# Kernel optimization log

Hardware: AMD Instinct MI355X
Metric: run time of the kernel (lower is better)

The kernel has to match this reference:

```python
import jax, jax.numpy as jnp
from jax import lax
import numpy as np

NF = 64   # nf
T = 7     # in_nc == 2*radius+1 frames
KS = 3    # deform kernel size
K = KS * KS


def conv2d(x, w, b, stride=1, pad=1):
    out = lax.conv_general_dilated(x, w, (stride, stride), [(pad, pad), (pad, pad)],
                                   dimension_numbers=('NCHW', 'OIHW', 'NCHW'))
    return out + b[None, :, None, None]


def convT2d(x, w, b):
    # torch ConvTranspose2d(k=4, stride=2, padding=1); w: (Cin, Cout, 4, 4)
    wf = jnp.flip(w, (2, 3)).transpose(1, 0, 2, 3)
    out = lax.conv_general_dilated(x, wf, (1, 1), [(2, 2), (2, 2)], lhs_dilation=(2, 2),
                                   dimension_numbers=('NCHW', 'OIHW', 'NCHW'))
    return out + b[None, :, None, None]


def bilinear_gather(img, ys, xs):
    # img: (C, H, W); ys/xs: (...,) absolute pixel coords; zero padding outside
    C, H, W = img.shape
    y0 = jnp.floor(ys); x0 = jnp.floor(xs)
    wy = ys - y0; wx = xs - x0

    def tap(yi, xi, wgt):
        valid = (yi >= 0) & (yi <= H - 1) & (xi >= 0) & (xi <= W - 1)
        yc = jnp.clip(yi, 0, H - 1).astype(jnp.int32)
        xc = jnp.clip(xi, 0, W - 1).astype(jnp.int32)
        return img[:, yc, xc] * (wgt * valid.astype(img.dtype))

    return (tap(y0, x0, (1 - wy) * (1 - wx)) + tap(y0, x0 + 1, (1 - wy) * wx)
            + tap(y0 + 1, x0, wy * (1 - wx)) + tap(y0 + 1, x0 + 1, wy * wx))


def flow_warp(x, flow):
    # x: (C, H, W); flow: (H, W, 2) with (dx, dy); align_corners=True grid_sample
    # with the normalization in the torch code reduces to absolute-pixel bilinear.
    H, W = x.shape[-2:]
    gy, gx = jnp.meshgrid(jnp.arange(H, dtype=x.dtype), jnp.arange(W, dtype=x.dtype), indexing='ij')
    return bilinear_gather(x, gy + flow[..., 1], gx + flow[..., 0])


def mod_deform_conv(x, off, msk, w, b):
    # Modulated deformable conv v2; deformable_groups = Cin (1 channel per group).
    B, Cin, H, W = x.shape
    G = Cin
    off = off.reshape(B, G, K, 2, H, W)   # per-group (dy, dx) per kernel tap
    msk = msk.reshape(B, G, K, H, W)
    gy, gx = jnp.meshgrid(jnp.arange(H, dtype=x.dtype), jnp.arange(W, dtype=x.dtype), indexing='ij')
    kk = jnp.arange(K)
    ky = (kk // KS - KS // 2).astype(x.dtype)
    kx = (kk % KS - KS // 2).astype(x.dtype)
    ys = gy[None, None, None] + ky[None, None, :, None, None] + off[:, :, :, 0]  # (B,G,K,H,W)
    xs = gx[None, None, None] + kx[None, None, :, None, None] + off[:, :, :, 1]
    xg = x.reshape(B, G, 1, H, W)
    samp = jax.vmap(jax.vmap(jax.vmap(bilinear_gather, in_axes=(None, 0, 0)),
                             in_axes=(0, 0, 0)), in_axes=(0, 0, 0))(xg, ys, xs)
    # samp: (B, G, K, 1, H, W)
    mod = samp * msk[:, :, :, None]
    wk = w.reshape(w.shape[0], G, 1, K)   # (O, G, Cpg=1, K)
    out = jnp.einsum('bgkchw,ogck->bohw', mod, wk)
    return out + b[None, :, None, None]


def _agg(feats, aligned, pred, ff_w, ff_b, dn1_w, dn1_b, dn2_w, dn2_b,
         tr_cw, tr_cb, tr_tw, tr_tb, up1_cw, up1_cb, up1_tw, up1_tb,
         up2_cw, up2_cb, up2_tw, up2_tb):
    B, T_, C, H, W = feats.shape
    ref = feats[:, T_ // 2][:, None]                      # center frame embedding
    p1 = jax.nn.sigmoid(aligned * ref)
    p2 = jax.nn.sigmoid(pred * ref)
    a1 = (aligned * p1).reshape(B, T_ * C, H, W)
    a2 = (pred * p2).reshape(B, T_ * C, H, W)
    f = feats.reshape(B, T_ * C, H, W)
    fuse = lambda z: jax.nn.leaky_relu(conv2d(z, ff_w, ff_b), 0.1)
    out0 = 0.1 * fuse(a1 + a2) + fuse(f)
    out1 = jax.nn.relu(conv2d(out0, dn1_w, dn1_b, stride=2))
    out2 = jax.nn.relu(conv2d(out1, dn2_w, dn2_b, stride=2))
    out = jax.nn.relu(convT2d(jax.nn.relu(conv2d(out2, tr_cw, tr_cb, stride=2)), tr_tw, tr_tb))
    out = jax.nn.relu(convT2d(jax.nn.relu(conv2d(jnp.concatenate([out, out2], 1), up2_cw, up2_cb)), up2_tw, up2_tb))
    out = jax.nn.relu(convT2d(jax.nn.relu(conv2d(jnp.concatenate([out, out1], 1), up1_cw, up1_cb)), up1_tw, up1_tb))
    return out


def _forward(lqs, preds, mv, bw1, bb1, bw2, bb2, dn1_w, dn1_b, dn2_w, dn2_b,
             up1_cw, up1_cb, up1_tw, up1_tb, up2_cw, up2_cb, up2_tw, up2_tb,
             tr_cw, tr_cb, tr_tw, tr_tb, ff_w, ff_b, om_w, om_b, dc_w, dc_b):
    B, T_, H, W = lqs.shape
    bb = lambda z: conv2d(conv2d(z, bw1, bb1), bw2, bb2)
    feat = bb(lqs.reshape(B * T_, 1, H, W)).reshape(B, T_, NF, H, W)
    pred_feat = bb(preds).reshape(B, T_, NF, H, W)
    # alg_MV_fea[:,0] = feat[:,0]; alg_MV_fea[:,i] = warp(feat[:,i-1], mv[:,i-1])
    prev = feat[:, :T_ - 1].reshape(B * (T_ - 1), NF, H, W)
    flows = mv.reshape(B * (T_ - 1), H, W, 2)
    warped = jax.vmap(flow_warp)(prev, flows).reshape(B, T_ - 1, NF, H, W)
    alg = jnp.concatenate([feat[:, :1], warped], axis=1)
    feat_f = _agg(feat, alg, pred_feat, ff_w, ff_b, dn1_w, dn1_b, dn2_w, dn2_b,
                  tr_cw, tr_cb, tr_tw, tr_tb, up1_cw, up1_cb, up1_tw, up1_tb,
                  up2_cw, up2_cb, up2_tw, up2_tb)
    off_msk = conv2d(feat_f, om_w, om_b)      # (B, T*3*K, H, W)
    n_off = T_ * 2 * K
    off = off_msk[:, :n_off]
    m = jax.nn.sigmoid(off_msk[:, n_off:])
    return jax.nn.relu(mod_deform_conv(lqs, off, m, dc_w, dc_b))


def setup_inputs():
    key = jax.random.key(0)
    ks = iter(jax.random.split(key, 40))
    B, H, W = 1, 192, 192
    r = lambda shape: jax.random.normal(next(ks), shape, jnp.float32)
    w = lambda shape: r(shape) * 0.05
    return {
        'lqs': r((B, T, H, W)),
        'preds': r((B * T, 1, H, W)),
        'mv': r((B, T - 1, H, W, 2)),
        'bw1': w((NF, 1, 3, 3)), 'bb1': w((NF,)),
        'bw2': w((NF, NF, 3, 3)), 'bb2': w((NF,)),
        'dn1_w': w((NF, NF, 3, 3)), 'dn1_b': w((NF,)),
        'dn2_w': w((NF, NF, 3, 3)), 'dn2_b': w((NF,)),
        'up1_cw': w((NF, 2 * NF, 3, 3)), 'up1_cb': w((NF,)),
        'up1_tw': w((NF, NF, 4, 4)), 'up1_tb': w((NF,)),
        'up2_cw': w((NF, 2 * NF, 3, 3)), 'up2_cb': w((NF,)),
        'up2_tw': w((NF, NF, 4, 4)), 'up2_tb': w((NF,)),
        'tr_cw': w((NF, NF, 3, 3)), 'tr_cb': w((NF,)),
        'tr_tw': w((NF, NF, 4, 4)), 'tr_tb': w((NF,)),
        'ff_w': w((NF, T * NF, 3, 3)), 'ff_b': w((NF,)),
        'om_w': w((T * 3 * K, NF, 3, 3)), 'om_b': w((T * 3 * K,)),
        'dc_w': w((NF, T, 3, 3)), 'dc_b': w((NF,)),
    }


def reference(lqs, preds, mv, bw1, bb1, bw2, bb2, dn1_w, dn1_b, dn2_w, dn2_b,
              up1_cw, up1_cb, up1_tw, up1_tb, up2_cw, up2_cb, up2_tw, up2_tb,
              tr_cw, tr_cb, tr_tw, tr_tb, ff_w, ff_b, om_w, om_b, dc_w, dc_b):
    return _forward(lqs, preds, mv, bw1, bb1, bw2, bb2, dn1_w, dn1_b, dn2_w, dn2_b,
                    up1_cw, up1_cb, up1_tw, up1_tb, up2_cw, up2_cb, up2_tw, up2_tb,
                    tr_cw, tr_cb, tr_tw, tr_tb, ff_w, ff_b, om_w, om_b, dc_w, dc_b)
```

## Files before the change

kernel.cpp:

```cpp
#include <hip/hip_runtime.h>
#include <math.h>

#define IMH 192
#define IMW 192
#define HWF 36864
#define PDIM 194

typedef unsigned short u16t;
typedef __attribute__((ext_vector_type(8))) short short8;
typedef __attribute__((ext_vector_type(4))) float f32x4;

__device__ __forceinline__ float sigmoidf(float x){ return 1.f/(1.f+expf(-x)); }
__device__ __forceinline__ float lrelu(float x){ return x > 0.f ? x : 0.1f*x; }
__device__ __forceinline__ float b2f(u16t h){ unsigned u = ((unsigned)h)<<16; return __uint_as_float(u); }
__device__ __forceinline__ u16t f2b(float f){
  unsigned u = __float_as_uint(f);
  u += 0x7FFFu + ((u>>16)&1u);
  return (u16t)(u>>16);
}

__device__ __forceinline__ float bilin(const float* __restrict__ img, float ys, float xs, int H, int W){
  float y0f = floorf(ys), x0f = floorf(xs);
  float wy = ys - y0f, wx = xs - x0f;
  int y0 = (int)y0f, x0 = (int)x0f;
  float acc = 0.f;
  #pragma unroll
  for (int dy=0; dy<2; ++dy){
    int yi = y0+dy;
    float wyv = dy ? wy : 1.f-wy;
    if (yi < 0 || yi >= H) continue;
    #pragma unroll
    for (int dx=0; dx<2; ++dx){
      int xi = x0+dx;
      float wxv = dx ? wx : 1.f-wx;
      if (xi < 0 || xi >= W) continue;
      acc += img[yi*W+xi]*(wyv*wxv);
    }
  }
  return acc;
}

struct PkD { const float* w; u16t* dst; int Cin, Cout, NT, total; };
struct PkD8 { PkD d[8]; };
__global__ __launch_bounds__(256) void pack_all(PkD8 ds){
  PkD d = ds.d[blockIdx.y];
  int id = blockIdx.x*256 + threadIdx.x;
  if (id >= d.total) return;
  int j = id & 7, l = (id>>3) & 63;
  int r = id >> 9;
  int nt = r % d.NT; r /= d.NT;
  int KC = d.Cin >> 5;
  int kc = r % KC; int tap = r / KC;
  int c = kc*32 + ((l>>4)<<3) + j;
  int o = nt*16 + (l&15);
  float v = (o < d.Cout) ? d.w[((size_t)o*d.Cin + c)*9 + tap] : 0.f;
  d.dst[id] = f2b(v);
}

struct RpD { const float* w; float* wp; };
struct RpD3 { RpD d[3]; };
__global__ __launch_bounds__(256) void repack_all(RpD3 ds){
  RpD d = ds.d[blockIdx.y];
  int id = blockIdx.x*256 + threadIdx.x;
  int par = id >> 12, o = (id >> 6) & 63, i = id & 63;
  int ry = par >> 1, rx = par & 1;
  #pragma unroll
  for (int jy = 0; jy < 2; ++jy)
    #pragma unroll
    for (int jx = 0; jx < 2; ++jx){
      int ka = 3 - ry - 2*jy, kb = 3 - rx - 2*jx;
      d.wp[((size_t)((par*64 + o)*64 + i))*4 + jy*2 + jx] = d.w[((size_t)(i*64 + o))*16 + ka*4 + kb];
    }
}

struct PzD { u16t* buf; int C, dim, nimg; size_t stride; };
struct PzD5 { PzD d[5]; };
__global__ __launch_bounds__(256) void padzero_all(PzD5 ds){
  PzD d = ds.d[blockIdx.y];
  int per = (4*d.dim - 4)*d.C;
  long total = (long)per*d.nimg;
  for (long id = (long)blockIdx.x*256 + threadIdx.x; id < total; id += (long)gridDim.x*256){
    int n = (int)(id / per), c2 = (int)(id % per);
    int cell = c2 / d.C, c = c2 % d.C;
    int d2 = d.dim - 1;
    int r, col;
    if (cell < d.dim){ r = 0; col = cell; }
    else if (cell < 2*d.dim){ r = d2; col = cell - d.dim; }
    else if (cell < 3*d.dim - 2){ r = cell - 2*d.dim + 1; col = 0; }
    else { r = cell - (3*d.dim - 2) + 1; col = d2; }
    d.buf[(size_t)n*d.stride + ((size_t)r*d.dim + col)*d.C + c] = 0;
  }
}

__global__ __launch_bounds__(256) void padzero2(u16t* buf, int C, int dim){
  int total = (4*dim - 4)*C;
  for (int id = blockIdx.x*256 + threadIdx.x; id < total; id += gridDim.x*256){
    int cell = id / C, c = id % C;
    int d2 = dim - 1;
    int r, col;
    if (cell < dim){ r = 0; col = cell; }
    else if (cell < 2*dim){ r = d2; col = cell - dim; }
    else if (cell < 3*dim - 2){ r = cell - 2*dim + 1; col = 0; }
    else { r = cell - (3*dim - 2) + 1; col = d2; }
    buf[((size_t)r*dim + col)*C + c] = 0;
  }
}

__global__ __launch_bounds__(256) void conv1_k(const float* __restrict__ lqs, const float* __restrict__ preds,
                                               const float* __restrict__ w,
                                               const float* __restrict__ bias, u16t* __restrict__ outp){
  __shared__ float sw[576];
  __shared__ float sb[64];
  int tid = threadIdx.x;
  for (int i = tid; i < 576; i += 256) sw[i] = w[i];
  if (tid < 64) sb[tid] = bias[tid];
  __syncthreads();
  int idx = blockIdx.x*256 + tid;
  int n = blockIdx.y;
  int y = idx/IMW, x = idx%IMW;
  const float* ip = (n < 7) ? (lqs + (size_t)n*HWF) : (preds + (size_t)(n-7)*HWF);
  float t[9];
  #pragma unroll
  for (int dy = 0; dy < 3; ++dy)
    #pragma unroll
    for (int dx = 0; dx < 3; ++dx){
      int yy = y+dy-1, xx = x+dx-1;
      t[dy*3+dx] = (yy>=0 && yy<IMH && xx>=0 && xx<IMW) ? ip[yy*IMW+xx] : 0.f;
    }
  u16t* op = outp + (size_t)n*(PDIM*PDIM*64) + ((size_t)(y+1)*PDIM + x+1)*64;
  #pragma unroll
  for (int o8 = 0; o8 < 8; ++o8){
    short8 ov;
    #pragma unroll
    for (int j = 0; j < 8; ++j){
      int o = o8*8 + j;
      float acc = sb[o];
      #pragma unroll
      for (int k = 0; k < 9; ++k) acc += t[k]*sw[o*9+k];
      ov[j] = (short)f2b(acc);
    }
    *(short8*)(op + o8*8) = ov;
  }
}

template<int STREAMS, int KC, int OMODE, int NTT, int SWZ>
__global__ __launch_bounds__(256) void cgemm(
    const u16t* __restrict__ A0, const u16t* __restrict__ A1,
    const u16t* __restrict__ Bp, const float* __restrict__ bias,
    float* __restrict__ outf, u16t* __restrict__ outb, u16t* __restrict__ outb2,
    int Cout, int blocksPerImg, int pitchIn, int csIn, size_t aImgStride, int KCtot)
{
  __shared__ u16t sA[STREAMS*108*40];
  int bid = blockIdx.x;
  if (SWZ) bid = (bid & 7)*(gridDim.x >> 3) + (bid >> 3);
  const int tid = threadIdx.x;
  const int wave = tid >> 6, lane = tid & 63;
  const int m = lane & 15, q = lane >> 4;
  const int img = bid / blocksPerImg;
  const int rem = bid - img*blocksPerImg;
  const int yg = rem / 12, xsg = rem % 12;
  const int y0 = yg*4, xs = xsg*16;
  const int rp = wave >> 1, np = wave & 1;
  const int ntB = (OMODE == 5) ? blockIdx.y*4 : 0;
  f32x4 acc[STREAMS][2][2];
  #pragma unroll
  for (int s = 0; s < STREAMS; ++s)
    #pragma unroll
    for (int r = 0; r < 2; ++r)
      #pragma unroll
      for (int n = 0; n < 2; ++n) acc[s][r][n] = (f32x4){0.f,0.f,0.f,0.f};

  #pragma unroll 1
  for (int kc = 0; kc < KC; ++kc){
    if (kc) __syncthreads();
    for (int u = tid; u < STREAMS*216; u += 256){
      int st = u/216, r2 = u%216, p = r2>>1, h = r2&1;
      int rr = p/18, cc = p%18;
      size_t ga = (size_t)img*aImgStride + ((size_t)(y0+rr)*pitchIn + xs+cc)*csIn + kc*32 + h*16;
      const u16t* gp = ((STREAMS==2 && st==1) ? A1 : A0) + ga;
      short8 v0 = *(const short8*)gp;
      short8 v1 = *(const short8*)(gp + 8);
      u16t* lp = &sA[((size_t)(st*108 + p))*40 + h*16];
      *(short8*)lp = v0;
      *(short8*)(lp+8) = v1;
    }
    __syncthreads();
    #pragma unroll
    for (int tap = 0; tap < 9; ++tap){
      const int dy = tap/3, dx = tap%3;
      short8 af[STREAMS][2];
      #pragma unroll
      for (int st = 0; st < STREAMS; ++st)
        #pragma unroll
        for (int r = 0; r < 2; ++r)
          af[st][r] = *(const short8*)&sA[((size_t)(st*108 + (2*rp + r + dy)*18 + dx + m))*40 + q*8];
      const u16t* bp = Bp + ((size_t)(tap*KCtot + kc)*NTT + ntB + np*2)*512 + lane*8;
      short8 b0 = *(const short8*)bp;
      short8 b1 = *(const short8*)(bp + 512);
      #pragma unroll
      for (int st = 0; st < STREAMS; ++st)
        #pragma unroll
        for (int r = 0; r < 2; ++r){
          acc[st][r][0] = __builtin_amdgcn_mfma_f32_16x16x32_bf16(af[st][r], b0, acc[st][r][0], 0, 0, 0);
          acc[st][r][1] = __builtin_amdgcn_mfma_f32_16x16x32_bf16(af[st][r], b1, acc[st][r][1], 0, 0, 0);
        }
    }
  }
  const int px0 = q*4;
  #pragma unroll
  for (int r = 0; r < 2; ++r){
    int yout = y0 + 2*rp + r;
    #pragma unroll
    for (int n = 0; n < 2; ++n){
      int oL = (np*2 + n)*16 + m;
      if (OMODE == 4){
        float bv = bias[oL];
        #pragma unroll
        for (int g = 0; g < 4; ++g){
          int px = xs + px0 + g;
          float v = 0.1f*lrelu(acc[0][r][n][g] + bv) + lrelu(acc[1][r][n][g] + bv);
          outb[((size_t)(yout+1)*PDIM + px+1)*64 + oL] = f2b(v);
        }
      } else if (OMODE == 5){
        int o = ntB*16 + oL;
        if (o < Cout){
          float bv = bias[o];
          #pragma unroll
          for (int g = 0; g < 4; ++g){
            int px = xs + px0 + g;
            outf[(size_t)o*HWF + (size_t)yout*IMW + px] = acc[0][r][n][g] + bv;
          }
        }
      } else {
        float bv = bias[oL];
        #pragma unroll
        for (int g = 0; g < 4; ++g){
          int px = xs + px0 + g;
          float v = acc[0][r][n][g] + bv;
          if (img < 7)
            outb[((size_t)(yout+1)*PDIM + px+1)*448 + (size_t)img*64 + oL] = f2b(v);
          else
            outb2[(size_t)(img-7)*((size_t)HWF*64) + ((size_t)yout*IMW + px)*64 + oL] = f2b(v);
        }
      }
    }
  }
}

template<int NT, int STREAMS, int KC, int STRIDE, int OMODE, int ACT, int SWZ>
__global__ __launch_bounds__(256) void gconv3(
    const u16t* __restrict__ A0, const u16t* __restrict__ A1,
    const u16t* __restrict__ Bp, const float* __restrict__ bias,
    float* __restrict__ outf, u16t* __restrict__ outb,
    int Cout, int Wout, int strips, int blocksPerImg,
    int pitchIn, int csIn, int coIn, size_t aImgStride,
    size_t outImgStride, int pitchOut, int csOut, int coOut,
    int KCtot, int NTtot)
{
  int bid = blockIdx.x;
  if (SWZ) bid = (bid & 7)*(gridDim.x >> 3) + (bid >> 3);
  const int wave = threadIdx.x >> 6;
  const int lane = threadIdx.x & 63;
  const int img = bid / blocksPerImg;
  const int sid = (bid - img*blocksPerImg)*4 + wave;
  const int y = sid / strips, xs = (sid % strips) * 16;
  const int m = lane & 15, q = lane >> 4;
  const int ntOff = blockIdx.y*NT;
  f32x4 acc[NT];
  #pragma unroll
  for (int nt = 0; nt < NT; ++nt) acc[nt] = (f32x4){0.f,0.f,0.f,0.f};

  for (int tap = 0; tap < 9; ++tap){
    int dy = tap/3, dx = tap%3;
    int row = STRIDE*y + dy;
    int col = (STRIDE == 1) ? (xs + m + dx) : (2*(xs + m) + dx);
    size_t abase = (size_t)img*aImgStride + ((size_t)row*pitchIn + col)*csIn + coIn + q*8;
    const u16t* ap0 = A0 + abase;
    const u16t* bp = Bp + ((size_t)(tap*KCtot)*NTtot + ntOff)*512 + lane*8;
    #pragma unroll
    for (int kc = 0; kc < KC; ++kc){
      short8 av0 = *(const short8*)(ap0 + kc*32);
      #pragma unroll
      for (int nt = 0; nt < NT; ++nt){
        short8 bv = *(const short8*)(bp + (size_t)(kc*NTtot + nt)*512);
        acc[nt] = __builtin_amdgcn_mfma_f32_16x16x32_bf16(av0, bv, acc[nt], 0, 0, 0);
      }
    }
  }
  const int prow0 = q*4;
  #pragma unroll
  for (int nt = 0; nt < NT; ++nt){
    int o = (ntOff + nt)*16 + m;
    if (o >= Cout) continue;
    float bv = bias[o];
    #pragma unroll
    for (int r = 0; r < 4; ++r){
      int px = xs + prow0 + r;
      if (px >= Wout) continue;
      float v = acc[nt][r] + bv;
      if (ACT) v = fmaxf(v, 0.f);
      if (OMODE == 0){
        outf[((size_t)img*Cout + o)*((size_t)Wout*Wout) + (size_t)y*Wout + px] = v;
      } else if (OMODE == 1){
        outb[(size_t)img*outImgStride + ((size_t)(y+1)*pitchOut + px+1)*csOut + coOut + o] = f2b(v);
      } else {
        outb[(size_t)img*outImgStride + ((size_t)y*pitchOut + px)*csOut + coOut + o] = f2b(v);
      }
    }
  }
}

__global__ __launch_bounds__(256) void gate_nhwc(
    const u16t* __restrict__ fpad, const u16t* __restrict__ pred,
    const float* __restrict__ mv, u16t* __restrict__ spad)
{
  int bid = blockIdx.x;
  int xcd = bid & 7;
  int k = bid >> 3;
  int t = k % 7;
  int lb = k / 7;
  int idx = (xcd*18 + lb)*256 + threadIdx.x;
  int y = idx/IMW, x = idx%IMW;
  size_t pc = ((size_t)(y+1)*PDIM + (x+1))*448;
  const u16t* rp = fpad + pc + 192;
  const u16t* pp = pred + ((size_t)t*HWF + idx)*64;
  u16t* sp = spad + pc + (size_t)t*64;
  const u16t* tp[4]; float tw[4];
  if (t == 0){
    tp[0] = fpad + pc; tw[0] = 1.f;
    tp[1] = tp[2] = tp[3] = fpad + pc; tw[1] = tw[2] = tw[3] = 0.f;
  } else {
    float fx = mv[(((size_t)(t-1)*HWF + idx))*2 + 0];
    float fy = mv[(((size_t)(t-1)*HWF + idx))*2 + 1];
    float ys = (float)y + fy, xs = (float)x + fx;
    float y0f = floorf(ys), x0f = floorf(xs);
    float wy = ys - y0f, wx = xs - x0f;
    int y0 = (int)y0f, x0i = (int)x0f;
    int kk = 0;
    #pragma unroll
    for (int dy2 = 0; dy2 < 2; ++dy2)
      #pragma unroll
      for (int dx2 = 0; dx2 < 2; ++dx2){
        int yi = y0+dy2, xi = x0i+dx2;
        float wv = (dy2 ? wy : 1.f-wy)*(dx2 ? wx : 1.f-wx);
        bool ok = (yi >= 0 && yi <= 191 && xi >= 0 && xi <= 191);
        int yc = min(max(yi,0),191), xc = min(max(xi,0),191);
        tp[kk] = fpad + ((size_t)(yc+1)*PDIM + xc+1)*448 + (size_t)(t-1)*64;
        tw[kk] = ok ? wv : 0.f;
        ++kk;
      }
  }
  #pragma unroll
  for (int c8 = 0; c8 < 8; ++c8){
    short8 rv = *(const short8*)(rp + c8*8);
    short8 pv = *(const short8*)(pp + c8*8);
    short8 t0v = *(const short8*)(tp[0] + c8*8);
    short8 t1v = *(const short8*)(tp[1] + c8*8);
    short8 t2v = *(const short8*)(tp[2] + c8*8);
    short8 t3v = *(const short8*)(tp[3] + c8*8);
    short8 ov;
    #pragma unroll
    for (int j = 0; j < 8; ++j){
      float r = b2f((u16t)rv[j]);
      float p = b2f((u16t)pv[j]);
      float a = tw[0]*b2f((u16t)t0v[j]) + tw[1]*b2f((u16t)t1v[j])
              + tw[2]*b2f((u16t)t2v[j]) + tw[3]*b2f((u16t)t3v[j]);
      float sv = a*sigmoidf(a*r) + p*sigmoidf(p*r);
      ov[j] = (short)f2b(sv);
    }
    *(short8*)(sp + c8*8) = ov;
  }
}

__global__ __launch_bounds__(256) void convT_tile2(
    const float* __restrict__ in, const float* __restrict__ wp,
    const float* __restrict__ bias, u16t* __restrict__ outb,
    int Hin, int tilesX, int pitchOut, int csOut, int coOut)
{
  const int CC = 4;
  __shared__ float sIn[CC][10*11];
  __shared__ float sW[16][CC][4][4];
  const int Win = Hin;
  const int o0 = blockIdx.x*16;
  const int tile = blockIdx.y;
  const int ty0 = (tile/tilesX)*16, tx0 = (tile%tilesX)*16;
  const int tid = threadIdx.x;
  const int py = tid>>4, px = tid&15;
  const int ry = py&1, rx = px&1, par = ry*2 + rx;
  const int lr = py>>1, lc = px>>1;
  const int r0 = ty0>>1, c0 = tx0>>1;
  float acc[16] = {};
  for (int ib = 0; ib < 64; ib += CC){
    for (int i = tid; i < CC*100; i += 256){
      int c = i/100, rem = i%100, r = rem/10, col = rem%10;
      int gy = r0 - 1 + r, gx = c0 - 1 + col;
      float v = 0.f;
      if (gy >= 0 && gy < Hin && gx >= 0 && gx < Win)
        v = in[(size_t)(ib + c)*Hin*Win + gy*Win + gx];
      sIn[c][r*11 + col] = v;
    }
    for (int i = tid; i < 1024; i += 256){
      int ol = i >> 6, rem = i & 63, ci = rem >> 4, p2 = (rem >> 2) & 3, j = rem & 3;
      sW[ol][ci][p2][j] = wp[((size_t)((p2*64 + o0 + ol)*64) + ib + ci)*4 + j];
    }
    __syncthreads();
    #pragma unroll
    for (int ci = 0; ci < CC; ++ci){
      int rb = lr + ry, cb = lc + rx;
      float t00 = sIn[ci][rb*11 + cb],     t01 = sIn[ci][rb*11 + cb + 1];
      float t10 = sIn[ci][(rb+1)*11 + cb], t11 = sIn[ci][(rb+1)*11 + cb + 1];
      #pragma unroll
      for (int ol = 0; ol < 16; ++ol){
        const float* wv = &sW[ol][ci][par][0];
        acc[ol] += t00*wv[0] + t01*wv[1] + t10*wv[2] + t11*wv[3];
      }
    }
    __syncthreads();
  }
  int gy = ty0 + py, gx = tx0 + px;
  u16t* op = outb + ((size_t)(gy+1)*pitchOut + gx+1)*csOut + coOut + o0;
  short8 pa, pb;
  #pragma unroll
  for (int i = 0; i < 8; ++i) pa[i] = (short)f2b(fmaxf(acc[i] + bias[o0+i], 0.f));
  #pragma unroll
  for (int i = 0; i < 8; ++i) pb[i] = (short)f2b(fmaxf(acc[8+i] + bias[o0+8+i], 0.f));
  *(short8*)op = pa;
  *(short8*)(op + 8) = pb;
}

__global__ __launch_bounds__(256) void deform_sample_k(
    const float* __restrict__ lqs, const float* __restrict__ om,
    float* __restrict__ vbuf)
{
  int idx = blockIdx.x*256 + threadIdx.x;
  int g = blockIdx.y;
  int h = idx / IMW, x = idx % IMW;
  const float* img = lqs + (size_t)g*HWF;
  #pragma unroll
  for (int k = 0; k < 9; ++k){
    int j = g*9 + k;
    float offy = om[(size_t)(j*2 + 0)*HWF + idx];
    float offx = om[(size_t)(j*2 + 1)*HWF + idx];
    float m = sigmoidf(om[(size_t)(126 + j)*HWF + idx]);
    float ys = (float)(h + (k/3) - 1) + offy;
    float xs = (float)(x + (k%3) - 1) + offx;
    vbuf[(size_t)j*HWF + idx] = bilin(img, ys, xs, IMH, IMW) * m;
  }
}

__global__ __launch_bounds__(256) void deform_out_k(
    const float* __restrict__ vbuf, const float* __restrict__ dcw,
    const float* __restrict__ dcb, float* __restrict__ out)
{
  __shared__ float sw[16*63];
  int idx = blockIdx.x*256 + threadIdx.x;
  int o0 = blockIdx.y*16;
  for (int i = threadIdx.x; i < 16*63; i += 256)
    sw[i] = dcw[(size_t)o0*63 + i];
  __syncthreads();
  float v[63];
  #pragma unroll
  for (int j = 0; j < 63; ++j) v[j] = vbuf[(size_t)j*HWF + idx];
  for (int ol = 0; ol < 16; ++ol){
    float acc = dcb[o0 + ol];
    #pragma unroll
    for (int j = 0; j < 63; ++j) acc += v[j]*sw[ol*63 + j];
    out[(size_t)(o0 + ol)*HWF + idx] = fmaxf(acc, 0.f);
  }
}

extern "C" void kernel_launch(void* const* d_in, const int* in_sizes, int n_in,
                              void* d_out, int out_size, void* d_ws, size_t ws_size,
                              hipStream_t stream)
{
  const float* lqs   = (const float*)d_in[0];
  const float* preds = (const float*)d_in[1];
  const float* mv    = (const float*)d_in[2];
  const float* bw1   = (const float*)d_in[3];
  const float* bb1   = (const float*)d_in[4];
  const float* bw2   = (const float*)d_in[5];
  const float* bb2   = (const float*)d_in[6];
  const float* dn1w  = (const float*)d_in[7];
  const float* dn1b  = (const float*)d_in[8];
  const float* dn2w  = (const float*)d_in[9];
  const float* dn2b  = (const float*)d_in[10];
  const float* up1cw = (const float*)d_in[11];
  const float* up1cb = (const float*)d_in[12];
  const float* up1tw = (const float*)d_in[13];
  const float* up1tb = (const float*)d_in[14];
  const float* up2cw = (const float*)d_in[15];
  const float* up2cb = (const float*)d_in[16];
  const float* up2tw = (const float*)d_in[17];
  const float* up2tb = (const float*)d_in[18];
  const float* trcw  = (const float*)d_in[19];
  const float* trcb  = (const float*)d_in[20];
  const float* trtw  = (const float*)d_in[21];
  const float* trtb  = (const float*)d_in[22];
  const float* ffw   = (const float*)d_in[23];
  const float* ffb   = (const float*)d_in[24];
  const float* omw   = (const float*)d_in[25];
  const float* omb   = (const float*)d_in[26];
  const float* dcw   = (const float*)d_in[27];
  const float* dcb   = (const float*)d_in[28];
  float* outp = (float*)d_out;

  char* p = (char*)d_ws;
  const size_t PIMG64 = (size_t)PDIM*PDIM*64;
  u16t* bbpad    = (u16t*)p; p += 14*PIMG64*2;
  u16t* fpad     = (u16t*)p; p += (size_t)PDIM*PDIM*448*2;
  u16t* prednhwc = (u16t*)p; p += (size_t)7*HWF*64*2;
  u16t* out0pad  = (u16t*)p; p += (size_t)PDIM*PDIM*64*2;
  u16t* cat1pad  = (u16t*)p; p += (size_t)98*98*128*2;
  u16t* cat2pad  = (u16t*)p; p += (size_t)50*50*128*2;
  float* t0      = (float*)p; p += (size_t)24*24*64*4;
  float* u2      = (float*)p; p += (size_t)48*48*64*4;
  float* u1      = (float*)p; p += (size_t)96*96*64*4;
  u16t* ffwpack  = (u16t*)p; p += 258048*2;
  u16t* c2pack   = (u16t*)p; p += 36864*2;
  u16t* ompack   = (u16t*)p; p += 110592*2;
  u16t* dn1pack  = (u16t*)p; p += 36864*2;
  u16t* dn2pack  = (u16t*)p; p += 36864*2;
  u16t* trcpack  = (u16t*)p; p += 36864*2;
  u16t* up2cpack = (u16t*)p; p += 73728*2;
  u16t* up1cpack = (u16t*)p; p += 73728*2;
  float* wp0     = (float*)p; p += 65536*4;
  float* wp1     = (float*)p; p += 65536*4;
  float* wp2     = (float*)p; p += 65536*4;

  u16t* spad = bbpad;
  u16t* featfpad = bbpad;
  float* om = (float*)prednhwc;
  float* vbuf = (float*)fpad;

  dim3 blk(256);
  PkD8 pk = {{ {ffw, ffwpack, 448, 64, 4, 258048}, {bw2, c2pack, 64, 64, 4, 36864},
               {omw, ompack, 64, 189, 12, 110592}, {dn1w, dn1pack, 64, 64, 4, 36864},
               {dn2w, dn2pack, 64, 64, 4, 36864},  {trcw, trcpack, 64, 64, 4, 36864},
               {up2cw, up2cpack, 128, 64, 4, 73728}, {up1cw, up1cpack, 128, 64, 4, 73728} }};
  pack_all<<<dim3(1008,8), blk, 0, stream>>>(pk);
  RpD3 rp3 = {{ {trtw, wp0}, {up2tw, wp1}, {up1tw, wp2} }};
  repack_all<<<dim3(64,3), blk, 0, stream>>>(rp3);
  PzD5 pz = {{ {bbpad, 64, PDIM, 14, PIMG64}, {fpad, 448, PDIM, 1, 0},
               {out0pad, 64, PDIM, 1, 0}, {cat1pad, 128, 98, 1, 0}, {cat2pad, 128, 50, 1, 0} }};
  padzero_all<<<dim3(2704,5), blk, 0, stream>>>(pz);
  conv1_k<<<dim3(144,14), blk, 0, stream>>>(lqs, preds, bw1, bb1, bbpad);
  cgemm<1,2,12,4,1><<<dim3(8064,1), blk, 0, stream>>>(bbpad, nullptr, c2pack, bb2,
      nullptr, fpad, prednhwc, 64, 576, PDIM, 64, PIMG64, 2);
  padzero2<<<dim3(1352), blk, 0, stream>>>(spad, 448, PDIM);
  gate_nhwc<<<dim3(1008), blk, 0, stream>>>(fpad, prednhwc, mv, spad);
  cgemm<2,14,4,4,1><<<dim3(576,1), blk, 0, stream>>>(spad, fpad, ffwpack, ffb,
      nullptr, out0pad, nullptr, 64, 576, PDIM, 448, 0, 14);
  gconv3<4,1,2,2,1,1,1><<<dim3(144,1), blk, 0, stream>>>(out0pad, nullptr, dn1pack, dn1b, nullptr, cat1pad,
      64, 96, 6, 144, PDIM, 64, 0, 0, 0, 98, 128, 64, 2, 4);
  gconv3<4,1,2,2,1,1,0><<<dim3(36,1), blk, 0, stream>>>(cat1pad, nullptr, dn2pack, dn2b, nullptr, cat2pad,
      64, 48, 3, 36, 98, 128, 64, 0, 0, 50, 128, 64, 2, 4);
  gconv3<4,1,2,2,0,1,0><<<dim3(12,1), blk, 0, stream>>>(cat2pad, nullptr, trcpack, trcb, t0, nullptr,
      64, 24, 2, 12, 50, 128, 64, 0, 0, 0, 0, 0, 2, 4);
  convT_tile2<<<dim3(4,9), blk, 0, stream>>>(t0, wp0, trtb, cat2pad, 24, 3, 50, 128, 0);
  gconv3<4,1,4,1,0,1,0><<<dim3(36,1), blk, 0, stream>>>(cat2pad, nullptr, up2cpack, up2cb, u2, nullptr,
      64, 48, 3, 36, 50, 128, 0, 0, 0, 0, 0, 0, 4, 4);
  convT_tile2<<<dim3(4,36), blk, 0, stream>>>(u2, wp1, up2tb, cat1pad, 48, 6, 98, 128, 0);
  gconv3<4,1,4,1,0,1,1><<<dim3(144,1), blk, 0, stream>>>(cat1pad, nullptr, up1cpack, up1cb, u1, nullptr,
      64, 96, 6, 144, 98, 128, 0, 0, 0, 0, 0, 0, 4, 4);
  padzero2<<<dim3(194), blk, 0, stream>>>(featfpad, 64, PDIM);
  convT_tile2<<<dim3(4,144), blk, 0, stream>>>(u1, wp2, up1tb, featfpad, 96, 12, PDIM, 64, 0);
  cgemm<1,2,5,12,1><<<dim3(576,3), blk, 0, stream>>>(featfpad, nullptr, ompack, omb,
      om, nullptr, nullptr, 189, 576, PDIM, 64, 0, 2);
  deform_sample_k<<<dim3(144,7), blk, 0, stream>>>(lqs, om, vbuf);
  deform_out_k<<<dim3(144,4), blk, 0, stream>>>(vbuf, dcw, dcb, outp);
}
```

Before: 659.5 us.

## Fuse first two backbone convs, loop gate over frames, split gconv3 over output tiles

New measurement: 604.7 us. 8.3% less time.

```diff
diff --git a/kernel.cpp b/kernel.cpp
--- a/kernel.cpp
+++ b/kernel.cpp
@@ -106,40 +106,102 @@
   }
 }
 
-__global__ __launch_bounds__(256) void conv1_k(const float* __restrict__ lqs, const float* __restrict__ preds,
-                                               const float* __restrict__ w,
-                                               const float* __restrict__ bias, u16t* __restrict__ outp){
-  __shared__ float sw[576];
-  __shared__ float sb[64];
-  int tid = threadIdx.x;
-  for (int i = tid; i < 576; i += 256) sw[i] = w[i];
-  if (tid < 64) sb[tid] = bias[tid];
+__global__ __launch_bounds__(256) void bbfused(
+    const float* __restrict__ lqs, const float* __restrict__ preds,
+    const float* __restrict__ w1, const float* __restrict__ b1,
+    const u16t* __restrict__ Bp, const float* __restrict__ b2,
+    u16t* __restrict__ fpad, u16t* __restrict__ prednhwc)
+{
+  __shared__ float sIn1[8][20];
+  __shared__ float sw1[576];
+  __shared__ float sb1[64];
+  __shared__ u16t sA[108*68];
+  int bid = blockIdx.x;
+  bid = (bid & 7)*(gridDim.x >> 3) + (bid >> 3);
+  const int tid = threadIdx.x;
+  const int img = bid / 576;
+  const int rem = bid - img*576;
+  const int y0 = (rem/12)*4, xs = (rem%12)*16;
+  for (int i = tid; i < 576; i += 256) sw1[i] = w1[i];
+  if (tid < 64) sb1[tid] = b1[tid];
+  const float* ip = (img < 7) ? (lqs + (size_t)img*HWF) : (preds + (size_t)(img-7)*HWF);
+  for (int u = tid; u < 160; u += 256){
+    int lr = u/20, lc = u%20;
+    int iy = y0 - 2 + lr, ix = xs - 2 + lc;
+    sIn1[lr][lc] = (iy >= 0 && iy < IMH && ix >= 0 && ix < IMW) ? ip[iy*IMW + ix] : 0.f;
+  }
   __syncthreads();
-  int idx = blockIdx.x*256 + tid;
-  int n = blockIdx.y;
-  int y = idx/IMW, x = idx%IMW;
-  const float* ip = (n < 7) ? (lqs + (size_t)n*HWF) : (preds + (size_t)(n-7)*HWF);
-  float t[9];
-  #pragma unroll
-  for (int dy = 0; dy < 3; ++dy)
-    #pragma unroll
-    for (int dx = 0; dx < 3; ++dx){
-      int yy = y+dy-1, xx = x+dx-1;
-      t[dy*3+dx] = (yy>=0 && yy<IMH && xx>=0 && xx<IMW) ? ip[yy*IMW+xx] : 0.f;
-    }
-  u16t* op = outp + (size_t)n*(PDIM*PDIM*64) + ((size_t)(y+1)*PDIM + x+1)*64;
-  #pragma unroll
-  for (int o8 = 0; o8 < 8; ++o8){
-    short8 ov;
-    #pragma unroll
-    for (int j = 0; j < 8; ++j){
-      int o = o8*8 + j;
-      float acc = sb[o];
-      #pragma unroll
-      for (int k = 0; k < 9; ++k) acc += t[k]*sw[o*9+k];
-      ov[j] = (short)f2b(acc);
-    }
-    *(short8*)(op + o8*8) = ov;
+  for (int u = tid; u < 216; u += 256){
+    int px = u >> 1, half = u & 1;
+    int rr = px/18, cc = px%18;
+    int pr = y0 + rr, pc = xs + cc;
+    bool border = (pr == 0) | (pr == 193) | (pc == 0) | (pc == 193);
+    float t[9];
+    #pragma unroll
+    for (int dy = 0; dy < 3; ++dy)
+      #pragma unroll
+      for (int dx = 0; dx < 3; ++dx) t[dy*3+dx] = sIn1[rr+dy][cc+dx];
+    #pragma unroll
+    for (int o8 = 0; o8 < 4; ++o8){
+      int ob = half*32 + o8*8;
+      short8 ov;
+      #pragma unroll
+      for (int j = 0; j < 8; ++j){
+        int o = ob + j;
+        float acc = sb1[o];
+        #pragma unroll
+        for (int k = 0; k < 9; ++k) acc += t[k]*sw1[o*9+k];
+        ov[j] = (short)(border ? (u16t)0 : f2b(acc));
+      }
+      *(short8*)&sA[(size_t)px*68 + ob] = ov;
+    }
+  }
+  __syncthreads();
+  const int wave = tid >> 6, lane = tid & 63;
+  const int m = lane & 15, q = lane >> 4;
+  const int rp = wave >> 1, np = wave & 1;
+  f32x4 acc[2][2];
+  #pragma unroll
+  for (int r = 0; r < 2; ++r)
+    #pragma unroll
+    for (int n = 0; n < 2; ++n) acc[r][n] = (f32x4){0.f,0.f,0.f,0.f};
+  #pragma unroll
+  for (int kc = 0; kc < 2; ++kc){
+    #pragma unroll
+    for (int tap = 0; tap < 9; ++tap){
+      const int dy = tap/3, dx = tap%3;
+      short8 af[2];
+      #pragma unroll
+      for (int r = 0; r < 2; ++r)
+        af[r] = *(const short8*)&sA[(size_t)((2*rp + r + dy)*18 + dx + m)*68 + kc*32 + q*8];
+      const u16t* bp = Bp + ((size_t)(tap*2 + kc)*4 + np*2)*512 + lane*8;
+      short8 b0 = *(const short8*)bp;
+      short8 b1v = *(const short8*)(bp + 512);
+      #pragma unroll
+      for (int r = 0; r < 2; ++r){
+        acc[r][0] = __builtin_amdgcn_mfma_f32_16x16x32_bf16(af[r], b0, acc[r][0], 0, 0, 0);
+        acc[r][1] = __builtin_amdgcn_mfma_f32_16x16x32_bf16(af[r], b1v, acc[r][1], 0, 0, 0);
+      }
+    }
+  }
+  const int px0 = q*4;
+  #pragma unroll
+  for (int r = 0; r < 2; ++r){
+    int yout = y0 + 2*rp + r;
+    #pragma unroll
+    for (int n = 0; n < 2; ++n){
+      int oL = (np*2 + n)*16 + m;
+      float bv = b2[oL];
+      #pragma unroll
+      for (int g = 0; g < 4; ++g){
+        int px = xs + px0 + g;
+        float v = acc[r][n][g] + bv;
+        if (img < 7)
+          fpad[((size_t)(yout+1)*PDIM + px+1)*448 + (size_t)img*64 + oL] = f2b(v);
+        else
+          prednhwc[(size_t)(img-7)*((size_t)HWF*64) + ((size_t)yout*IMW + px)*64 + oL] = f2b(v);
+      }
+    }
   }
 }
 
@@ -158,8 +220,7 @@
   const int m = lane & 15, q = lane >> 4;
   const int img = bid / blocksPerImg;
   const int rem = bid - img*blocksPerImg;
-  const int yg = rem / 12, xsg = rem % 12;
-  const int y0 = yg*4, xs = xsg*16;
+  const int y0 = (rem/12)*4, xs = (rem%12)*16;
   const int rp = wave >> 1, np = wave & 1;
   const int ntB = (OMODE == 5) ? blockIdx.y*4 : 0;
   f32x4 acc[STREAMS][2][2];
@@ -221,7 +282,7 @@
           float v = 0.1f*lrelu(acc[0][r][n][g] + bv) + lrelu(acc[1][r][n][g] + bv);
           outb[((size_t)(yout+1)*PDIM + px+1)*64 + oL] = f2b(v);
         }
-      } else if (OMODE == 5){
+      } else {
         int o = ntB*16 + oL;
         if (o < Cout){
           float bv = bias[o];
@@ -231,26 +292,14 @@
             outf[(size_t)o*HWF + (size_t)yout*IMW + px] = acc[0][r][n][g] + bv;
           }
         }
-      } else {
-        float bv = bias[oL];
-        #pragma unroll
-        for (int g = 0; g < 4; ++g){
-          int px = xs + px0 + g;
-          float v = acc[0][r][n][g] + bv;
-          if (img < 7)
-            outb[((size_t)(yout+1)*PDIM + px+1)*448 + (size_t)img*64 + oL] = f2b(v);
-          else
-            outb2[(size_t)(img-7)*((size_t)HWF*64) + ((size_t)yout*IMW + px)*64 + oL] = f2b(v);
-        }
-      }
-    }
-  }
-}
-
-template<int NT, int STREAMS, int KC, int STRIDE, int OMODE, int ACT, int SWZ>
+      }
+    }
+  }
+}
+
+template<int NT, int KC, int STRIDE, int OMODE, int ACT, int SWZ>
 __global__ __launch_bounds__(256) void gconv3(
-    const u16t* __restrict__ A0, const u16t* __restrict__ A1,
-    const u16t* __restrict__ Bp, const float* __restrict__ bias,
+    const u16t* __restrict__ A0, const u16t* __restrict__ Bp, const float* __restrict__ bias,
     float* __restrict__ outf, u16t* __restrict__ outb,
     int Cout, int Wout, int strips, int blocksPerImg,
     int pitchIn, int csIn, int coIn, size_t aImgStride,
@@ -315,60 +364,62 @@
     const float* __restrict__ mv, u16t* __restrict__ spad)
 {
   int bid = blockIdx.x;
-  int xcd = bid & 7;
-  int k = bid >> 3;
-  int t = k % 7;
-  int lb = k / 7;
+  int xcd = bid & 7, lb = bid >> 3;
   int idx = (xcd*18 + lb)*256 + threadIdx.x;
   int y = idx/IMW, x = idx%IMW;
   size_t pc = ((size_t)(y+1)*PDIM + (x+1))*448;
   const u16t* rp = fpad + pc + 192;
-  const u16t* pp = pred + ((size_t)t*HWF + idx)*64;
-  u16t* sp = spad + pc + (size_t)t*64;
-  const u16t* tp[4]; float tw[4];
-  if (t == 0){
-    tp[0] = fpad + pc; tw[0] = 1.f;
-    tp[1] = tp[2] = tp[3] = fpad + pc; tw[1] = tw[2] = tw[3] = 0.f;
-  } else {
-    float fx = mv[(((size_t)(t-1)*HWF + idx))*2 + 0];
-    float fy = mv[(((size_t)(t-1)*HWF + idx))*2 + 1];
-    float ys = (float)y + fy, xs = (float)x + fx;
-    float y0f = floorf(ys), x0f = floorf(xs);
-    float wy = ys - y0f, wx = xs - x0f;
-    int y0 = (int)y0f, x0i = (int)x0f;
-    int kk = 0;
-    #pragma unroll
-    for (int dy2 = 0; dy2 < 2; ++dy2)
-      #pragma unroll
-      for (int dx2 = 0; dx2 < 2; ++dx2){
-        int yi = y0+dy2, xi = x0i+dx2;
-        float wv = (dy2 ? wy : 1.f-wy)*(dx2 ? wx : 1.f-wx);
-        bool ok = (yi >= 0 && yi <= 191 && xi >= 0 && xi <= 191);
-        int yc = min(max(yi,0),191), xc = min(max(xi,0),191);
-        tp[kk] = fpad + ((size_t)(yc+1)*PDIM + xc+1)*448 + (size_t)(t-1)*64;
-        tw[kk] = ok ? wv : 0.f;
-        ++kk;
-      }
-  }
-  #pragma unroll
-  for (int c8 = 0; c8 < 8; ++c8){
-    short8 rv = *(const short8*)(rp + c8*8);
-    short8 pv = *(const short8*)(pp + c8*8);
-    short8 t0v = *(const short8*)(tp[0] + c8*8);
-    short8 t1v = *(const short8*)(tp[1] + c8*8);
-    short8 t2v = *(const short8*)(tp[2] + c8*8);
-    short8 t3v = *(const short8*)(tp[3] + c8*8);
-    short8 ov;
-    #pragma unroll
-    for (int j = 0; j < 8; ++j){
-      float r = b2f((u16t)rv[j]);
-      float p = b2f((u16t)pv[j]);
-      float a = tw[0]*b2f((u16t)t0v[j]) + tw[1]*b2f((u16t)t1v[j])
-              + tw[2]*b2f((u16t)t2v[j]) + tw[3]*b2f((u16t)t3v[j]);
-      float sv = a*sigmoidf(a*r) + p*sigmoidf(p*r);
-      ov[j] = (short)f2b(sv);
-    }
-    *(short8*)(sp + c8*8) = ov;
+  short8 r8[8];
+  #pragma unroll
+  for (int c8 = 0; c8 < 8; ++c8) r8[c8] = *(const short8*)(rp + c8*8);
+  #pragma unroll 1
+  for (int t = 0; t < 7; ++t){
+    const u16t* pp = pred + ((size_t)t*HWF + idx)*64;
+    u16t* sp = spad + pc + (size_t)t*64;
+    const u16t* tp[4]; float tw[4];
+    if (t == 0){
+      tp[0] = fpad + pc; tw[0] = 1.f;
+      tp[1] = tp[2] = tp[3] = fpad + pc; tw[1] = tw[2] = tw[3] = 0.f;
+    } else {
+      float fx = mv[(((size_t)(t-1)*HWF + idx))*2 + 0];
+      float fy = mv[(((size_t)(t-1)*HWF + idx))*2 + 1];
+      float ys = (float)y + fy, xsf = (float)x + fx;
+      float y0f = floorf(ys), x0f = floorf(xsf);
+      float wy = ys - y0f, wx = xsf - x0f;
+      int y0 = (int)y0f, x0i = (int)x0f;
+      int kk = 0;
+      #pragma unroll
+      for (int dy2 = 0; dy2 < 2; ++dy2)
+        #pragma unroll
+        for (int dx2 = 0; dx2 < 2; ++dx2){
+          int yi = y0+dy2, xi = x0i+dx2;
+          float wv = (dy2 ? wy : 1.f-wy)*(dx2 ? wx : 1.f-wx);
+          bool ok = (yi >= 0 && yi <= 191 && xi >= 0 && xi <= 191);
+          int yc = min(max(yi,0),191), xc = min(max(xi,0),191);
+          tp[kk] = fpad + ((size_t)(yc+1)*PDIM + xc+1)*448 + (size_t)(t-1)*64;
+          tw[kk] = ok ? wv : 0.f;
+          ++kk;
+        }
+    }
+    #pragma unroll
+    for (int c8 = 0; c8 < 8; ++c8){
+      short8 pv = *(const short8*)(pp + c8*8);
+      short8 t0v = *(const short8*)(tp[0] + c8*8);
+      short8 t1v = *(const short8*)(tp[1] + c8*8);
+      short8 t2v = *(const short8*)(tp[2] + c8*8);
+      short8 t3v = *(const short8*)(tp[3] + c8*8);
+      short8 ov;
+      #pragma unroll
+      for (int j = 0; j < 8; ++j){
+        float r = b2f((u16t)r8[c8][j]);
+        float p = b2f((u16t)pv[j]);
+        float a = tw[0]*b2f((u16t)t0v[j]) + tw[1]*b2f((u16t)t1v[j])
+                + tw[2]*b2f((u16t)t2v[j]) + tw[3]*b2f((u16t)t3v[j]);
+        float sv = a*sigmoidf(a*r) + p*sigmoidf(p*r);
+        ov[j] = (short)f2b(sv);
+      }
+      *(short8*)(sp + c8*8) = ov;
+    }
   }
 }
 
@@ -506,7 +557,7 @@
 
   char* p = (char*)d_ws;
   const size_t PIMG64 = (size_t)PDIM*PDIM*64;
-  u16t* bbpad    = (u16t*)p; p += 14*PIMG64*2;
+  u16t* spadreg  = (u16t*)p; p += 14*PIMG64*2;
   u16t* fpad     = (u16t*)p; p += (size_t)PDIM*PDIM*448*2;
   u16t* prednhwc = (u16t*)p; p += (size_t)7*HWF*64*2;
   u16t* out0pad  = (u16t*)p; p += (size_t)PDIM*PDIM*64*2;
@@ -527,8 +578,8 @@
   float* wp1     = (float*)p; p += 65536*4;
   float* wp2     = (float*)p; p += 65536*4;
 
-  u16t* spad = bbpad;
-  u16t* featfpad = bbpad;
+  u16t* spad = spadreg;
+  u16t* featfpad = spadreg;
   float* om = (float*)prednhwc;
   float* vbuf = (float*)fpad;
 
@@ -540,27 +591,24 @@
   pack_all<<<dim3(1008,8), blk, 0, stream>>>(pk);
   RpD3 rp3 = {{ {trtw, wp0}, {up2tw, wp1}, {up1tw, wp2} }};
   repack_all<<<dim3(64,3), blk, 0, stream>>>(rp3);
-  PzD5 pz = {{ {bbpad, 64, PDIM, 14, PIMG64}, {fpad, 448, PDIM, 1, 0},
+  PzD5 pz = {{ {spad, 448, PDIM, 1, 0}, {fpad, 448, PDIM, 1, 0},
                {out0pad, 64, PDIM, 1, 0}, {cat1pad, 128, 98, 1, 0}, {cat2pad, 128, 50, 1, 0} }};
   padzero_all<<<dim3(2704,5), blk, 0, stream>>>(pz);
-  conv1_k<<<dim3(144,14), blk, 0, stream>>>(lqs, preds, bw1, bb1, bbpad);
-  cgemm<1,2,12,4,1><<<dim3(8064,1), blk, 0, stream>>>(bbpad, nullptr, c2pack, bb2,
-      nullptr, fpad, prednhwc, 64, 576, PDIM, 64, PIMG64, 2);
-  padzero2<<<dim3(1352), blk, 0, stream>>>(spad, 448, PDIM);
-  gate_nhwc<<<dim3(1008), blk, 0, stream>>>(fpad, prednhwc, mv, spad);
+  bbfused<<<dim3(8064), blk, 0, stream>>>(lqs, preds, bw1, bb1, c2pack, bb2, fpad, prednhwc);
+  gate_nhwc<<<dim3(144), blk, 0, stream>>>(fpad, prednhwc, mv, spad);
   cgemm<2,14,4,4,1><<<dim3(576,1), blk, 0, stream>>>(spad, fpad, ffwpack, ffb,
       nullptr, out0pad, nullptr, 64, 576, PDIM, 448, 0, 14);
-  gconv3<4,1,2,2,1,1,1><<<dim3(144,1), blk, 0, stream>>>(out0pad, nullptr, dn1pack, dn1b, nullptr, cat1pad,
+  gconv3<1,2,2,1,1,1><<<dim3(144,4), blk, 0, stream>>>(out0pad, dn1pack, dn1b, nullptr, cat1pad,
       64, 96, 6, 144, PDIM, 64, 0, 0, 0, 98, 128, 64, 2, 4);
-  gconv3<4,1,2,2,1,1,0><<<dim3(36,1), blk, 0, stream>>>(cat1pad, nullptr, dn2pack, dn2b, nullptr, cat2pad,
+  gconv3<1,2,2,1,1,0><<<dim3(36,4), blk, 0, stream>>>(cat1pad, dn2pack, dn2b, nullptr, cat2pad,
       64, 48, 3, 36, 98, 128, 64, 0, 0, 50, 128, 64, 2, 4);
-  gconv3<4,1,2,2,0,1,0><<<dim3(12,1), blk, 0, stream>>>(cat2pad, nullptr, trcpack, trcb, t0, nullptr,
+  gconv3<1,2,2,0,1,0><<<dim3(12,4), blk, 0, stream>>>(cat2pad, trcpack, trcb, t0, nullptr,
       64, 24, 2, 12, 50, 128, 64, 0, 0, 0, 0, 0, 2, 4);
   convT_tile2<<<dim3(4,9), blk, 0, stream>>>(t0, wp0, trtb, cat2pad, 24, 3, 50, 128, 0);
-  gconv3<4,1,4,1,0,1,0><<<dim3(36,1), blk, 0, stream>>>(cat2pad, nullptr, up2cpack, up2cb, u2, nullptr,
+  gconv3<1,4,1,0,1,0><<<dim3(36,4), blk, 0, stream>>>(cat2pad, up2cpack, up2cb, u2, nullptr,
       64, 48, 3, 36, 50, 128, 0, 0, 0, 0, 0, 0, 4, 4);
   convT_tile2<<<dim3(4,36), blk, 0, stream>>>(u2, wp1, up2tb, cat1pad, 48, 6, 98, 128, 0);
-  gconv3<4,1,4,1,0,1,1><<<dim3(144,1), blk, 0, stream>>>(cat1pad, nullptr, up1cpack, up1cb, u1, nullptr,
+  gconv3<1,4,1,0,1,1><<<dim3(144,4), blk, 0, stream>>>(cat1pad, up1cpack, up1cb, u1, nullptr,
       64, 96, 6, 144, 98, 128, 0, 0, 0, 0, 0, 0, 4, 4);
   padzero2<<<dim3(194), blk, 0, stream>>>(featfpad, 64, PDIM);
   convT_tile2<<<dim3(4,144), blk, 0, stream>>>(u1, wp2, up1tb, featfpad, 96, 12, PDIM, 64, 0);
```
